# Kernel optimization log

Hardware: AMD Instinct MI355X
Metric: run time of the kernel (lower is better)

The kernel has to match this reference:

```python
import jax, jax.numpy as jnp
import numpy as np

N_HEAD = 16
BLOCK_SIZE = 2049  # w2 last dim = block_size - 1 = 2048


def setup_inputs() -> dict:
    key = jax.random.key(0)
    ks = jax.random.split(key, 9)
    B, T, C = 2, 2048, 1024
    hd = C // N_HEAD
    M = BLOCK_SIZE - 1
    return {
        "x": jax.random.normal(ks[0], (B, T, C), jnp.float32),
        "w1_w": jax.random.normal(ks[1], (C, C), jnp.float32) * 0.02,
        "w1_b": jax.random.normal(ks[2], (C,), jnp.float32) * 0.02,
        # torch uniform_(a=-0.001, b=0.001)
        "w2": jax.random.uniform(ks[3], (N_HEAD, hd, M), jnp.float32, -0.001, 0.001),
        "b2": jax.random.normal(ks[4], (M,), jnp.float32) * 0.02,
        "value_w": jax.random.normal(ks[5], (C, C), jnp.float32) * 0.02,
        "value_b": jax.random.normal(ks[6], (C,), jnp.float32) * 0.02,
        "proj_w": jax.random.normal(ks[7], (C, C), jnp.float32) * 0.02,
        "proj_b": jax.random.normal(ks[8], (C,), jnp.float32) * 0.02,
    }


def reference(x, w1_w, w1_b, w2, b2, value_w, value_b, proj_w, proj_b):
    B, T, C = x.shape
    H = N_HEAD
    hd = C // H
    M = w2.shape[-1]  # block_size - 1
    # kernel = relu(w1(x)), split heads -> [B, H, T, hd]
    k = jax.nn.relu(x @ w1_w.T + w1_b).reshape(B, T, H, hd).transpose(0, 2, 1, 3)
    # synthesizer scores: [B, H, T, M]
    attn = jnp.einsum('bhtd,hdm->bhtm', k, w2) + b2
    # causal mask = tril(ones(block,block))[:T, :M] == 0 -> -inf
    causal = jnp.tril(jnp.ones((T, M), dtype=bool))
    attn = jnp.where(causal, attn, -jnp.inf)
    # softmax over first T score columns
    attn = jax.nn.softmax(attn[..., :T], axis=-1)  # [B, H, T, T]
    v = (x @ value_w.T + value_b).reshape(B, T, H, hd).transpose(0, 2, 1, 3)
    out = jnp.einsum('bhts,bhsd->bhtd', attn, v)
    out = out.transpose(0, 2, 1, 3).reshape(B, T, C)
    return out @ proj_w.T + proj_b
```

## Files before the change

kernel.cpp:

```cpp
#include <hip/hip_runtime.h>
#include <math.h>
#include <stdint.h>

typedef __bf16 bf16;
typedef __bf16 bf16x8 __attribute__((ext_vector_type(8)));
typedef __bf16 bf16x4 __attribute__((ext_vector_type(4)));
typedef float f32x4 __attribute__((ext_vector_type(4)));
typedef unsigned int u32;

__device__ __forceinline__ int swz(int row, int chunk) {
    return row * 64 + ((chunk ^ (row & 7)) << 3);
}

__device__ __forceinline__ void gld16(void* lds, const void* g) {
    __builtin_amdgcn_global_load_lds(
        (const __attribute__((address_space(1))) u32*)g,
        (__attribute__((address_space(3))) u32*)lds, 16, 0, 0);
}

__device__ __forceinline__ void stage8(bf16* dst, const bf16* src, size_t srcStride,
                                       int w, int l) {
    const int br = w * 8;
    const int r = br + (l >> 3);
    const int gs = (l & 7) ^ (r & 7);
    gld16(dst + br * 64, src + (size_t)r * srcStride + gs * 8);
}

__global__ void cast_bf16_k(const float* __restrict__ src, bf16* __restrict__ dst, int n) {
    const int stride = gridDim.x * blockDim.x * 4;
    for (int i = (blockIdx.x * blockDim.x + threadIdx.x) * 4; i < n; i += stride) {
        float4 v = *(const float4*)(src + i);
        bf16x4 o = {(bf16)v.x, (bf16)v.y, (bf16)v.z, (bf16)v.w};
        *(bf16x4*)(dst + i) = o;
    }
}

__global__ void cast3_bf16_k(const float* __restrict__ s0, bf16* __restrict__ d0,
                             const float* __restrict__ s1, bf16* __restrict__ d1,
                             const float* __restrict__ s2, bf16* __restrict__ d2, int n) {
    const int stride = gridDim.x * blockDim.x * 4;
    for (int i = (blockIdx.x * blockDim.x + threadIdx.x) * 4; i < n; i += stride) {
        float4 v0 = *(const float4*)(s0 + i);
        float4 v1 = *(const float4*)(s1 + i);
        float4 v2 = *(const float4*)(s2 + i);
        bf16x4 o0 = {(bf16)v0.x, (bf16)v0.y, (bf16)v0.z, (bf16)v0.w};
        bf16x4 o1 = {(bf16)v1.x, (bf16)v1.y, (bf16)v1.z, (bf16)v1.w};
        bf16x4 o2 = {(bf16)v2.x, (bf16)v2.y, (bf16)v2.z, (bf16)v2.w};
        *(bf16x4*)(d0 + i) = o0;
        *(bf16x4*)(d1 + i) = o1;
        *(bf16x4*)(d2 + i) = o2;
    }
}

__global__ __launch_bounds__(256) void w2_transpose_k(const float* __restrict__ w2,
                                                      bf16* __restrict__ w2t, int M) {
    __shared__ float Tf[64][65];
    const int h = blockIdx.y, m0 = blockIdx.x * 64, t = threadIdx.x;
    {
        const int dr = t >> 4, c4 = (t & 15) * 4;
        #pragma unroll
        for (int it = 0; it < 4; ++it) {
            const int d = dr + it * 16;
            float4 v = *(const float4*)(w2 + ((size_t)h * 64 + d) * M + m0 + c4);
            Tf[d][c4] = v.x; Tf[d][c4 + 1] = v.y; Tf[d][c4 + 2] = v.z; Tf[d][c4 + 3] = v.w;
        }
    }
    __syncthreads();
    const int m = t >> 2;
    #pragma unroll
    for (int it = 0; it < 2; ++it) {
        const int ch = (t & 3) + it * 4;
        bf16x8 o;
        #pragma unroll
        for (int j = 0; j < 8; ++j) o[j] = (bf16)Tf[ch * 8 + j][m];
        *(bf16x8*)(w2t + ((size_t)h * M + m0 + m) * 64 + ch * 8) = o;
    }
}

__global__ __launch_bounds__(256) void gemm_bf16_k(const bf16* __restrict__ A,
                                                   const bf16* __restrict__ Bw,
                                                   const float* __restrict__ bias,
                                                   const float* __restrict__ bias2,
                                                   float* __restrict__ C0,
                                                   bf16* __restrict__ CK,
                                                   bf16* __restrict__ CV,
                                                   int M, int N, int K, int mode, int Ns)
{
    __shared__ __align__(16) bf16 As[128 * 64];
    __shared__ __align__(16) bf16 Bs[128 * 64];
    const int tid = threadIdx.x;
    const int w = tid >> 6, l = tid & 63;
    const int wr = w >> 1, wc = w & 1;
    const int lc = l & 15, lg = l >> 4;
    const int row0 = blockIdx.y * 128, col0 = blockIdx.x * 128;

    f32x4 acc[4][4] = {};

    for (int k0 = 0; k0 < K; k0 += 64) {
        __syncthreads();
        #pragma unroll
        for (int i = 0; i < 4; ++i) {
            const int br = (w * 4 + i) * 8;
            const int r = br + (l >> 3);
            const int gs = (l & 7) ^ (r & 7);
            gld16(As + br * 64, A  + (size_t)(row0 + r) * K + k0 + gs * 8);
            gld16(Bs + br * 64, Bw + (size_t)(col0 + r) * K + k0 + gs * 8);
        }
        __syncthreads();
        #pragma unroll
        for (int ks = 0; ks < 2; ++ks) {
            bf16x8 af[4], bfv[4];
            #pragma unroll
            for (int i = 0; i < 4; ++i) {
                af[i]  = *(const bf16x8*)&As[swz(wr * 64 + i * 16 + lc, ks * 4 + lg)];
                bfv[i] = *(const bf16x8*)&Bs[swz(wc * 64 + i * 16 + lc, ks * 4 + lg)];
            }
            #pragma unroll
            for (int mi = 0; mi < 4; ++mi)
                #pragma unroll
                for (int ni = 0; ni < 4; ++ni)
                    acc[mi][ni] = __builtin_amdgcn_mfma_f32_16x16x32_bf16(af[mi], bfv[ni], acc[mi][ni], 0, 0, 0);
        }
    }

    #pragma unroll
    for (int ni = 0; ni < 4; ++ni) {
        const int col = col0 + wc * 64 + ni * 16 + lc;
        #pragma unroll
        for (int mi = 0; mi < 4; ++mi) {
            const int rowb = row0 + wr * 64 + mi * 16 + lg * 4;
            f32x4 v = acc[mi][ni];
            if (mode == 0) {
                const float bv = bias[col];
                #pragma unroll
                for (int r = 0; r < 4; ++r)
                    C0[(size_t)(rowb + r) * N + col] = v[r] + bv;
            } else if (col < Ns) {
                const float bv = bias[col];
                #pragma unroll
                for (int r = 0; r < 4; ++r)
                    CK[(size_t)(rowb + r) * Ns + col] = (bf16)fmaxf(v[r] + bv, 0.f);
            } else {
                const float bv = bias2[col - Ns];
                const int b = rowb >> 11, tt = rowb & 2047;
                bf16x4 o = {(bf16)(v[0] + bv), (bf16)(v[1] + bv),
                            (bf16)(v[2] + bv), (bf16)(v[3] + bv)};
                *(bf16x4*)(CV + ((size_t)b * Ns + (col - Ns)) * 2048 + tt) = o;
            }
        }
    }
}

__device__ __forceinline__ void tile_step(bf16x8 kf0, bf16x8 kf1,
                                          const bf16* Wb, const bf16* Vb,
                                          bf16* Pw, const float* b2l, int s0,
                                          f32x4 (&acc)[4], float (&lsum)[4],
                                          bool diag, int lc, int lg, int wq)
{
    float bb[4];
    #pragma unroll
    for (int st = 0; st < 4; ++st) bb[st] = b2l[s0 + st * 16 + lc];
    f32x4 sv[4];
    #pragma unroll
    for (int st = 0; st < 4; ++st) sv[st] = {bb[st], bb[st], bb[st], bb[st]};
    #pragma unroll
    for (int st = 0; st < 4; ++st) {
        bf16x8 wb0 = *(const bf16x8*)&Wb[swz(st * 16 + lc, lg)];
        bf16x8 wb1 = *(const bf16x8*)&Wb[swz(st * 16 + lc, 4 + lg)];
        sv[st] = __builtin_amdgcn_mfma_f32_16x16x32_bf16(kf0, wb0, sv[st], 0, 0, 0);
        sv[st] = __builtin_amdgcn_mfma_f32_16x16x32_bf16(kf1, wb1, sv[st], 0, 0, 0);
    }
    #pragma unroll
    for (int st = 0; st < 4; ++st) {
        const int scol = st * 16 + lc;
        #pragma unroll
        for (int r = 0; r < 4; ++r) {
            float e = __expf(sv[st][r]);
            if (diag && scol > wq * 16 + lg * 4 + r) e = 0.f;
            lsum[r] += e;
            const int trow = lg * 4 + r;
            Pw[trow * 64 + (((scol >> 3) ^ (trow & 7)) << 3) + (scol & 7)] = (bf16)e;
        }
    }
    #pragma unroll
    for (int ks = 0; ks < 2; ++ks) {
        bf16x8 pf = *(const bf16x8*)&Pw[swz(lc, ks * 4 + lg)];
        #pragma unroll
        for (int dt = 0; dt < 4; ++dt) {
            bf16x8 vv = *(const bf16x8*)&Vb[swz(dt * 16 + lc, ks * 4 + lg)];
            acc[dt] = __builtin_amdgcn_mfma_f32_16x16x32_bf16(pf, vv, acc[dt], 0, 0, 0);
        }
    }
}

__global__ __launch_bounds__(512, 4) void synth_attn_v8(const bf16* __restrict__ Kb,
                                                        const bf16* __restrict__ VT,
                                                        const bf16* __restrict__ w2t,
                                                        const float* __restrict__ b2,
                                                        bf16* __restrict__ Ob)
{
    constexpr int T = 2048, C = 1024, M = 2048;
    __shared__ __align__(16) bf16 Wl[3][64 * 64];
    __shared__ __align__(16) bf16 Vl[3][64 * 64];
    __shared__ __align__(16) bf16 Pl[8][16 * 64];
    __shared__ float b2l[M];
    const int tid = threadIdx.x;
    const int w = tid >> 6, l = tid & 63;
    const int lc = l & 15, lg = l >> 4;
    const int wq = w & 3, wt = w >> 2;

    const int bx = blockIdx.x;
    const int j = bx & 15;
    const int bh = bx >> 4;
    const int h = bh & 15, b = bh >> 4;
    const int tA = j, tB = 31 - j;
    const int myT = wt ? tA : tB;
    const int t0 = myT * 64;

    *(float4*)&b2l[tid * 4] = *(const float4*)(b2 + tid * 4);
    __syncthreads();

    const bf16* Wgt = w2t + (size_t)h * M * 64;
    const bf16* Vgt = VT + ((size_t)b * C + h * 64) * T;
    bf16* Pw = &Pl[w][0];

    const bf16* Kg = Kb + (size_t)(b * T + t0 + wq * 16 + lc) * C + h * 64;
    const bf16x8 kf0 = *(const bf16x8*)(Kg + lg * 8);
    const bf16x8 kf1 = *(const bf16x8*)(Kg + 32 + lg * 8);

    stage8(&Wl[0][0], Wgt, 64, w, l);
    stage8(&Vl[0][0], Vgt, T, w, l);
    stage8(&Wl[1][0], Wgt + (size_t)64 * 64, 64, w, l);
    stage8(&Vl[1][0], Vgt + 64, T, w, l);

    f32x4 acc[4] = {};
    float lsum[4] = {0.f, 0.f, 0.f, 0.f};

    int cur = 0;
    for (int sb = 0; sb <= tB; ++sb) {
        const int s0 = sb * 64;
        if (sb < tB) asm volatile("s_waitcnt vmcnt(2)" ::: "memory");
        else         asm volatile("s_waitcnt vmcnt(0)" ::: "memory");
        __builtin_amdgcn_s_barrier();

        if (sb <= myT)
            tile_step(kf0, kf1, &Wl[cur][0], &Vl[cur][0], Pw, b2l, s0,
                      acc, lsum, sb == myT, lc, lg, wq);

        if (sb + 2 <= tB) {
            int nx = cur + 2; if (nx >= 3) nx -= 3;
            stage8(&Wl[nx][0], Wgt + (size_t)(s0 + 128) * 64, 64, w, l);
            stage8(&Vl[nx][0], Vgt + (s0 + 128), T, w, l);
        }
        if (++cur == 3) cur = 0;
    }

    #pragma unroll
    for (int r = 0; r < 4; ++r) {
        float ls = lsum[r];
        ls += __shfl_xor(ls, 1); ls += __shfl_xor(ls, 2);
        ls += __shfl_xor(ls, 4); ls += __shfl_xor(ls, 8);
        const float inv = 1.f / ls;
        bf16* dst = Ob + (size_t)(b * T + t0 + wq * 16 + lg * 4 + r) * C + h * 64;
        #pragma unroll
        for (int dt = 0; dt < 4; ++dt)
            dst[dt * 16 + lc] = (bf16)(acc[dt][r] * inv);
    }
}

extern "C" void kernel_launch(void* const* d_in, const int* in_sizes, int n_in,
                              void* d_out, int out_size, void* d_ws, size_t ws_size,
                              hipStream_t stream) {
    const float* x       = (const float*)d_in[0];
    const float* w1_w    = (const float*)d_in[1];
    const float* w1_b    = (const float*)d_in[2];
    const float* w2      = (const float*)d_in[3];
    const float* b2      = (const float*)d_in[4];
    const float* value_w = (const float*)d_in[5];
    const float* value_b = (const float*)d_in[6];
    const float* proj_w  = (const float*)d_in[7];
    const float* proj_b  = (const float*)d_in[8];

    const int B = 2, T = 2048, C = 1024, H = 16, M = 2048;
    const int R = B * T;

    bf16* xb  = (bf16*)d_ws;
    bf16* w1b = xb  + (size_t)R * C;
    bf16* vwb = w1b + (size_t)C * C;
    bf16* w2t = vwb + (size_t)C * C;
    bf16* pwb = w2t + (size_t)H * M * 64;
    bf16* Kb  = pwb + (size_t)C * C;
    bf16* VTb = Kb  + (size_t)R * C;
    bf16* Ob  = VTb + (size_t)R * C;

    cast_bf16_k<<<1024, 256, 0, stream>>>(x, xb, R * C);
    cast3_bf16_k<<<512, 256, 0, stream>>>(w1_w, w1b, value_w, vwb, proj_w, pwb, C * C);
    w2_transpose_k<<<dim3(M / 64, H), 256, 0, stream>>>(w2, w2t, M);

    gemm_bf16_k<<<dim3(2 * C / 128, R / 128), 256, 0, stream>>>(
        xb, w1b, w1_b, value_b, nullptr, Kb, VTb, R, 2 * C, C, 1, C);

    synth_attn_v8<<<dim3(512), 512, 0, stream>>>(Kb, VTb, w2t, b2, Ob);

    gemm_bf16_k<<<dim3(C / 128, R / 128), 256, 0, stream>>>(
        Ob, pwb, proj_b, nullptr, (float*)d_out, nullptr, nullptr, R, C, C, 0, C);
}
```

Baseline: 111.5 us.

## Double-buffer GEMM LDS tiles and transpose score MFMA in attention kernel

```diff
diff --git a/kernel.cpp b/kernel.cpp
--- a/kernel.cpp
+++ b/kernel.cpp
@@ -77,7 +77,7 @@
     }
 }
 
-__global__ __launch_bounds__(256) void gemm_bf16_k(const bf16* __restrict__ A,
+__global__ __launch_bounds__(256, 2) void gemm_bf16_k(const bf16* __restrict__ A,
                                                    const bf16* __restrict__ Bw,
                                                    const float* __restrict__ bias,
                                                    const float* __restrict__ bias2,
@@ -86,8 +86,8 @@
                                                    bf16* __restrict__ CV,
                                                    int M, int N, int K, int mode, int Ns)
 {
-    __shared__ __align__(16) bf16 As[128 * 64];
-    __shared__ __align__(16) bf16 Bs[128 * 64];
+    __shared__ __align__(16) bf16 As[2][128 * 64];
+    __shared__ __align__(16) bf16 Bs[2][128 * 64];
     const int tid = threadIdx.x;
     const int w = tid >> 6, l = tid & 63;
     const int wr = w >> 1, wc = w & 1;
@@ -96,24 +96,35 @@
 
     f32x4 acc[4][4] = {};
 
-    for (int k0 = 0; k0 < K; k0 += 64) {
-        __syncthreads();
+    const int nk = K >> 6;
+    auto issue = [&](int buf, int k0) {
         #pragma unroll
         for (int i = 0; i < 4; ++i) {
             const int br = (w * 4 + i) * 8;
             const int r = br + (l >> 3);
             const int gs = (l & 7) ^ (r & 7);
-            gld16(As + br * 64, A  + (size_t)(row0 + r) * K + k0 + gs * 8);
-            gld16(Bs + br * 64, Bw + (size_t)(col0 + r) * K + k0 + gs * 8);
-        }
-        __syncthreads();
+            gld16(&As[buf][br * 64], A  + (size_t)(row0 + r) * K + k0 + gs * 8);
+            gld16(&Bs[buf][br * 64], Bw + (size_t)(col0 + r) * K + k0 + gs * 8);
+        }
+    };
+
+    issue(0, 0);
+    int cur = 0;
+    for (int kt = 0; kt < nk; ++kt) {
+        if (kt + 1 < nk) {
+            issue(cur ^ 1, (kt + 1) << 6);
+            asm volatile("s_waitcnt vmcnt(8)" ::: "memory");
+        } else {
+            asm volatile("s_waitcnt vmcnt(0)" ::: "memory");
+        }
+        __builtin_amdgcn_s_barrier();
         #pragma unroll
         for (int ks = 0; ks < 2; ++ks) {
             bf16x8 af[4], bfv[4];
             #pragma unroll
             for (int i = 0; i < 4; ++i) {
-                af[i]  = *(const bf16x8*)&As[swz(wr * 64 + i * 16 + lc, ks * 4 + lg)];
-                bfv[i] = *(const bf16x8*)&Bs[swz(wc * 64 + i * 16 + lc, ks * 4 + lg)];
+                af[i]  = *(const bf16x8*)&As[cur][swz(wr * 64 + i * 16 + lc, ks * 4 + lg)];
+                bfv[i] = *(const bf16x8*)&Bs[cur][swz(wc * 64 + i * 16 + lc, ks * 4 + lg)];
             }
             #pragma unroll
             for (int mi = 0; mi < 4; ++mi)
@@ -121,6 +132,9 @@
                 for (int ni = 0; ni < 4; ++ni)
                     acc[mi][ni] = __builtin_amdgcn_mfma_f32_16x16x32_bf16(af[mi], bfv[ni], acc[mi][ni], 0, 0, 0);
         }
+        asm volatile("s_waitcnt lgkmcnt(0)" ::: "memory");
+        __builtin_amdgcn_s_barrier();
+        cur ^= 1;
     }
 
     #pragma unroll
@@ -154,33 +168,37 @@
 __device__ __forceinline__ void tile_step(bf16x8 kf0, bf16x8 kf1,
                                           const bf16* Wb, const bf16* Vb,
                                           bf16* Pw, const float* b2l, int s0,
-                                          f32x4 (&acc)[4], float (&lsum)[4],
+                                          f32x4 (&acc)[4], float& lsum,
                                           bool diag, int lc, int lg, int wq)
 {
-    float bb[4];
-    #pragma unroll
-    for (int st = 0; st < 4; ++st) bb[st] = b2l[s0 + st * 16 + lc];
     f32x4 sv[4];
     #pragma unroll
-    for (int st = 0; st < 4; ++st) sv[st] = {bb[st], bb[st], bb[st], bb[st]};
+    for (int st = 0; st < 4; ++st) {
+        const float4 b4 = *(const float4*)&b2l[s0 + st * 16 + lg * 4];
+        sv[st] = {b4.x, b4.y, b4.z, b4.w};
+    }
     #pragma unroll
     for (int st = 0; st < 4; ++st) {
         bf16x8 wb0 = *(const bf16x8*)&Wb[swz(st * 16 + lc, lg)];
         bf16x8 wb1 = *(const bf16x8*)&Wb[swz(st * 16 + lc, 4 + lg)];
-        sv[st] = __builtin_amdgcn_mfma_f32_16x16x32_bf16(kf0, wb0, sv[st], 0, 0, 0);
-        sv[st] = __builtin_amdgcn_mfma_f32_16x16x32_bf16(kf1, wb1, sv[st], 0, 0, 0);
-    }
+        sv[st] = __builtin_amdgcn_mfma_f32_16x16x32_bf16(wb0, kf0, sv[st], 0, 0, 0);
+        sv[st] = __builtin_amdgcn_mfma_f32_16x16x32_bf16(wb1, kf1, sv[st], 0, 0, 0);
+    }
+    const int qv = wq * 16 + lc;
     #pragma unroll
     for (int st = 0; st < 4; ++st) {
-        const int scol = st * 16 + lc;
+        float e[4];
         #pragma unroll
         for (int r = 0; r < 4; ++r) {
-            float e = __expf(sv[st][r]);
-            if (diag && scol > wq * 16 + lg * 4 + r) e = 0.f;
-            lsum[r] += e;
-            const int trow = lg * 4 + r;
-            Pw[trow * 64 + (((scol >> 3) ^ (trow & 7)) << 3) + (scol & 7)] = (bf16)e;
-        }
+            const int sidx = st * 16 + lg * 4 + r;
+            float ev = __expf(sv[st][r]);
+            if (diag && sidx > qv) ev = 0.f;
+            e[r] = ev;
+            lsum += ev;
+        }
+        bf16x4 pw = {(bf16)e[0], (bf16)e[1], (bf16)e[2], (bf16)e[3]};
+        const int chunk = st * 2 + (lg >> 1);
+        *(bf16x4*)&Pw[lc * 64 + ((chunk ^ (lc & 7)) << 3) + ((lg & 1) << 2)] = pw;
     }
     #pragma unroll
     for (int ks = 0; ks < 2; ++ks) {
@@ -193,7 +211,7 @@
     }
 }
 
-__global__ __launch_bounds__(512, 4) void synth_attn_v8(const bf16* __restrict__ Kb,
+__global__ __launch_bounds__(512, 4) void synth_attn_v9(const bf16* __restrict__ Kb,
                                                         const bf16* __restrict__ VT,
                                                         const bf16* __restrict__ w2t,
                                                         const float* __restrict__ b2,
@@ -234,7 +252,7 @@
     stage8(&Vl[1][0], Vgt + 64, T, w, l);
 
     f32x4 acc[4] = {};
-    float lsum[4] = {0.f, 0.f, 0.f, 0.f};
+    float lsum = 0.f;
 
     int cur = 0;
     for (int sb = 0; sb <= tB; ++sb) {
@@ -255,12 +273,12 @@
         if (++cur == 3) cur = 0;
     }
 
+    float ls = lsum;
+    ls += __shfl_xor(ls, 16);
+    ls += __shfl_xor(ls, 32);
     #pragma unroll
     for (int r = 0; r < 4; ++r) {
-        float ls = lsum[r];
-        ls += __shfl_xor(ls, 1); ls += __shfl_xor(ls, 2);
-        ls += __shfl_xor(ls, 4); ls += __shfl_xor(ls, 8);
-        const float inv = 1.f / ls;
+        const float inv = 1.f / __shfl(ls, lg * 4 + r);
         bf16* dst = Ob + (size_t)(b * T + t0 + wq * 16 + lg * 4 + r) * C + h * 64;
         #pragma unroll
         for (int dt = 0; dt < 4; ++dt)
@@ -300,7 +318,7 @@
     gemm_bf16_k<<<dim3(2 * C / 128, R / 128), 256, 0, stream>>>(
         xb, w1b, w1_b, value_b, nullptr, Kb, VTb, R, 2 * C, C, 1, C);
 
-    synth_attn_v8<<<dim3(512), 512, 0, stream>>>(Kb, VTb, w2t, b2, Ob);
+    synth_attn_v9<<<dim3(512), 512, 0, stream>>>(Kb, VTb, w2t, b2, Ob);
 
     gemm_bf16_k<<<dim3(C / 128, R / 128), 256, 0, stream>>>(
         Ob, pwb, proj_b, nullptr, (float*)d_out, nullptr, nullptr, R, C, C, 0, C);
```

Measured after the change: 103.2 us. -7.4%, faster.
